# Kernel tuning notes

Hardware: AMD Instinct MI355X
Metric: run time of the kernel (lower is better)

Reference implementation:

```python
import jax, jax.numpy as jnp
import numpy as np

HID = 256        # constant.hidden_size
EMB = 256        # constant.embedding_size
STATE_NUM = 5    # constant.state_num
PAD_ID = 0


def _lstm(x, Wih, Whh, b):
    # x: (N, T, D) -> (N, T, H); single-layer unidirectional, PyTorch gate order i,f,g,o
    N = x.shape[0]
    Hh = Whh.shape[1]
    def step(carry, xt):
        h, c = carry
        g = xt @ Wih.T + h @ Whh.T + b
        i, f, gg, o = jnp.split(g, 4, axis=-1)
        c = jax.nn.sigmoid(f) * c + jax.nn.sigmoid(i) * jnp.tanh(gg)
        h = jax.nn.sigmoid(o) * jnp.tanh(c)
        return (h, c), h
    h0 = jnp.zeros((N, Hh), x.dtype)
    _, ys = jax.lax.scan(step, (h0, h0), jnp.swapaxes(x, 0, 1))
    return jnp.swapaxes(ys, 0, 1)


def setup_inputs() -> dict:
    rng = np.random.RandomState(0)
    B, L, W, V = 8, 128, 48, 50000
    S = STATE_NUM
    P = L // (S - 1)
    batch_utterances = jnp.asarray(rng.randint(0, V, size=(B, L, W)), jnp.int32)
    utterance_sequence_length = jnp.asarray(rng.randint(1, W + 1, size=(B, L)), jnp.int32)
    perm = np.stack([b * L + rng.permutation(L) for b in range(B)]).reshape(-1)
    session_transpose_matrix = jnp.asarray(perm, jnp.int32)
    stm = np.zeros((B, L, S), np.int32)  # col 0 == 0 -> new-state slot (projection path)
    carry = rng.rand(B, L, S - 1) < 0.3
    pos = rng.randint(1, P + 1, size=(B, L, S - 1))
    stm[:, :, 1:] = np.where(carry, -1, pos)
    state_transition_matrix = jnp.asarray(stm)

    def w(*shape):
        return jnp.asarray(rng.randn(*shape) * 0.05, jnp.float32)

    return dict(
        batch_utterances=batch_utterances,
        utterance_sequence_length=utterance_sequence_length,
        session_transpose_matrix=session_transpose_matrix,
        state_transition_matrix=state_transition_matrix,
        max_conversation_length=L,
        emb=w(V, EMB),
        utt_Wih=w(4 * HID, EMB), utt_Whh=w(4 * HID, HID), utt_b=w(4 * HID),
        ws1=w(HID, HID), ws2=w(1, HID),
        conv_Wih=w(4 * HID, HID), conv_Whh=w(4 * HID, HID), conv_b=w(4 * HID),
        sess_Wih=w(4 * HID, HID), sess_Whh=w(4 * HID, HID), sess_b=w(4 * HID),
        Wp=w(HID, 2 * HID), bp=w(HID),
        Ws=w(HID, 2 * HID), bs=w(HID),
    )


def reference(batch_utterances, utterance_sequence_length, session_transpose_matrix,
              state_transition_matrix, max_conversation_length,
              emb, utt_Wih, utt_Whh, utt_b, ws1, ws2,
              conv_Wih, conv_Whh, conv_b, sess_Wih, sess_Whh, sess_b,
              Wp, bp, Ws, bs):
    B, L, W = batch_utterances.shape
    S = STATE_NUM
    P = L // (S - 1)
    Lc = int(max_conversation_length)

    # --- UtteranceEncoder: embedding lookup + word-level LSTM ---
    tok = batch_utterances.reshape(-1, W)            # (B*L, W)
    word_out = _lstm(emb[tok], utt_Wih, utt_Whh, utt_b)  # (B*L, W, H)

    # --- SelfAttentiveEncoder (1 hop) ---
    hbar = jnp.tanh(word_out @ ws1.T)                # (B*L, W, H)
    logits = (hbar @ ws2.T)[..., 0]                  # (B*L, W)
    logits = logits + (-10000.0) * (tok == PAD_ID).astype(logits.dtype)
    alphas = jax.nn.softmax(logits, axis=1)
    att = jnp.einsum('nw,nwh->nh', alphas, word_out).reshape(B, L, HID)

    # --- ConversationEncoder ---
    conv = _lstm(att, conv_Wih, conv_Whh, conv_b)    # (B, L, H)

    # --- SessionEncoder: gather-permute utterances into sessions, LSTM per session ---
    flat = att.reshape(-1, HID)[session_transpose_matrix]       # (B*L, H)
    sess_in = flat.reshape(B * (S - 1), P, HID)
    sess_out = _lstm(sess_in, sess_Wih, sess_Whh, sess_b).reshape(B, S - 1, P, HID)

    # --- StateMatrixEncoder: sequential scatter/gather scan over conversation steps ---
    sess_idx = jnp.clip(jnp.arange(S) - 1, 0, S - 2)            # (S,)
    gathered = sess_out[:, sess_idx]                            # (B, S, P, H)
    conv_shift = jnp.concatenate([conv[:, :1], conv[:, :L - 1]], axis=1)  # conv_repre[i-1] (i==0 -> [0])
    stm_T = jnp.swapaxes(state_transition_matrix, 0, 1)         # (L, B, S)
    cs_T = jnp.swapaxes(conv_shift, 0, 1)                       # (L, B, H)

    def step(prev_row, inp):
        stm_i, cs = inp                                         # (B,S), (B,H)
        posn = jnp.clip(stm_i - 1, 0, P - 1)
        v_g = jnp.take_along_axis(gathered, posn[:, :, None, None], axis=2)[:, :, 0, :]  # (B,S,H)
        is_carry = (stm_i == -1)[..., None]
        is_gather = (stm_i > 0)[..., None]
        v = jnp.where(is_carry, prev_row, jnp.where(is_gather, v_g, 0.0))
        # AvgPool2d((S-1,1)) over exactly S-1 collected vectors == masked mean
        one_res = jnp.sum(jnp.where(stm_i[..., None] != 0, v, 0.0), axis=1) / (S - 1)
        new0 = jax.nn.relu(jnp.concatenate([one_res, cs], axis=-1) @ Wp.T + bp)
        row = jnp.where(is_gather, v_g, 0.0).at[:, 0, :].set(new0)
        return row, row

    _, rows = jax.lax.scan(step, jnp.zeros((B, S, HID), att.dtype), (stm_T, cs_T))
    state_matrix = jnp.swapaxes(rows, 0, 1)                     # (B, L, S, H)

    # --- ScoresCalculator (unidirectional -> LogSoftmax) ---
    uc = jnp.concatenate([att[:, :Lc], conv[:, :Lc]], axis=-1)  # (B, Lc, 2H)
    up = jax.nn.relu(uc @ Ws.T + bs)                            # (B, Lc, H)
    scores = jnp.einsum('blsh,blh->bls', state_matrix[:, :Lc], up)
    return jax.nn.log_softmax(scores, axis=2)
```

## Files before the change

kernel.cpp:

```cpp
#include <hip/hip_runtime.h>
#include <hip/hip_bf16.h>
#include <math.h>

#define HIDN 256
#define GATES 1024
#define LLEN 128
#define WLEN 48
#define SNUM 5
#define PLEN 32
#define EMBD 256

typedef _Float16 f16;
typedef _Float16 h2_t __attribute__((ext_vector_type(2)));
typedef short short8_t __attribute__((ext_vector_type(8)));
typedef float f32x4 __attribute__((ext_vector_type(4)));

__device__ __forceinline__ float sigf(float x){ return 1.0f/(1.0f+expf(-x)); }

__device__ __forceinline__ unsigned short f2bf(float f){
  unsigned int x = __builtin_bit_cast(unsigned int, f);
  x += 0x7fffu + ((x >> 16) & 1u);
  return (unsigned short)(x >> 16);
}
__device__ __forceinline__ float bf2f(unsigned short u){
  unsigned int x = ((unsigned int)u) << 16;
  return __builtin_bit_cast(float, x);
}

__device__ __forceinline__ float fd2(unsigned int w, unsigned int h, float acc){
  h2_t wa = __builtin_bit_cast(h2_t, w);
  h2_t hb = __builtin_bit_cast(h2_t, h);
#if defined(__has_builtin)
#if __has_builtin(__builtin_amdgcn_fdot2)
  return __builtin_amdgcn_fdot2(wa, hb, acc, false);
#else
  return acc + (float)wa[0]*(float)hb[0] + (float)wa[1]*(float)hb[1];
#endif
#else
  return acc + (float)wa[0]*(float)hb[0] + (float)wa[1]*(float)hb[1];
#endif
}
__device__ __forceinline__ float dot8(uint4 w, uint4 h, float acc){
  acc = fd2(w.x, h.x, acc);
  acc = fd2(w.y, h.y, acc);
  acc = fd2(w.z, h.z, acc);
  acc = fd2(w.w, h.w, acc);
  return acc;
}

template<bool GATHER, bool BIAS, bool RELU, bool SPLIT>
__global__ __launch_bounds__(256) void gemm_abt64_k(
  const float* __restrict__ A, const float* __restrict__ A2,
  const float* __restrict__ Bm, const float* __restrict__ bias,
  float* __restrict__ C, const int* __restrict__ gidx,
  int K, int N, int ostride)
{
  __shared__ float As[32][68];
  __shared__ float Bs[32][68];
  const int tid = threadIdx.x;
  const int m0 = blockIdx.x*64, n0 = blockIdx.y*64;
  const int tx = tid & 15, ty = tid >> 4;
  const int lr = tid >> 3;
  const int lc = (tid & 7) * 4;
  float acc[4][4] = {};
  for (int k0 = 0; k0 < K; k0 += 32){
    #pragma unroll
    for (int hf = 0; hf < 2; ++hf){
      const int r = lr + hf*32;
      int am = m0 + r;
      if (GATHER) am = gidx[am];
      const float* asrc;
      if (SPLIT){
        if (k0 < 256) asrc = A  + (size_t)am*256 + k0 + lc;
        else          asrc = A2 + (size_t)am*256 + (k0-256) + lc;
      } else {
        asrc = A + (size_t)am*K + k0 + lc;
      }
      float4 av = *reinterpret_cast<const float4*>(asrc);
      float4 bv = *reinterpret_cast<const float4*>(Bm + (size_t)(n0+r)*K + k0 + lc);
      As[lc+0][r]=av.x; As[lc+1][r]=av.y; As[lc+2][r]=av.z; As[lc+3][r]=av.w;
      Bs[lc+0][r]=bv.x; Bs[lc+1][r]=bv.y; Bs[lc+2][r]=bv.z; Bs[lc+3][r]=bv.w;
    }
    __syncthreads();
    #pragma unroll
    for (int kk = 0; kk < 32; ++kk){
      const float4 a = *reinterpret_cast<const float4*>(&As[kk][ty*4]);
      const float4 b = *reinterpret_cast<const float4*>(&Bs[kk][tx*4]);
      acc[0][0] += a.x*b.x; acc[0][1] += a.x*b.y; acc[0][2] += a.x*b.z; acc[0][3] += a.x*b.w;
      acc[1][0] += a.y*b.x; acc[1][1] += a.y*b.y; acc[1][2] += a.y*b.z; acc[1][3] += a.y*b.w;
      acc[2][0] += a.z*b.x; acc[2][1] += a.z*b.y; acc[2][2] += a.z*b.z; acc[2][3] += a.z*b.w;
      acc[3][0] += a.w*b.x; acc[3][1] += a.w*b.y; acc[3][2] += a.w*b.z; acc[3][3] += a.w*b.w;
    }
    __syncthreads();
  }
  float4 bb;
  if (BIAS) bb = *reinterpret_cast<const float4*>(bias + n0 + tx*4);
  else      { bb.x=0.f; bb.y=0.f; bb.z=0.f; bb.w=0.f; }
  #pragma unroll
  for (int i = 0; i < 4; ++i){
    float4 o;
    o.x = acc[i][0]+bb.x; o.y = acc[i][1]+bb.y; o.z = acc[i][2]+bb.z; o.w = acc[i][3]+bb.w;
    if (RELU){ o.x=fmaxf(o.x,0.f); o.y=fmaxf(o.y,0.f); o.z=fmaxf(o.z,0.f); o.w=fmaxf(o.w,0.f); }
    *reinterpret_cast<float4*>(C + (size_t)(m0+ty*4+i)*ostride + n0 + tx*4) = o;
  }
}

__global__ __launch_bounds__(256) void cvt2_k(
  const float* __restrict__ a, const float* __restrict__ b,
  unsigned short* __restrict__ oa, unsigned short* __restrict__ ob, int n)
{
  for (int i = blockIdx.x*256 + threadIdx.x; i < n; i += gridDim.x*256){
    oa[i] = f2bf(a[i]);
    ob[i] = f2bf(b[i]);
  }
}
__global__ __launch_bounds__(256) void cvt1_k(
  const float* __restrict__ a, unsigned short* __restrict__ o, int n)
{
  for (int i = blockIdx.x*256 + threadIdx.x; i < n; i += gridDim.x*256)
    o[i] = f2bf(a[i]);
}
__global__ __launch_bounds__(256) void cvt_w16_k(
  const float* __restrict__ a, const float* __restrict__ b,
  f16* __restrict__ oa, f16* __restrict__ ob)
{
  const int i = blockIdx.x*256 + threadIdx.x;
  oa[i] = (f16)a[i];
  ob[i] = (f16)b[i];
}

__global__ __launch_bounds__(256) void remap_k(const int* __restrict__ tok, int* __restrict__ gidx2){
  const int idx = blockIdx.x*256 + threadIdx.x;
  const int t = idx >> 10, u = idx & 1023;
  gidx2[idx] = tok[u*WLEN + t];
}

template<int AMODE>
__global__ __launch_bounds__(256) void mmabt_k(
  const void* __restrict__ Asrc, const unsigned short* __restrict__ Wb,
  const float* __restrict__ bias, const int* __restrict__ gidx,
  float* __restrict__ Cout)
{
  __shared__ char As[32768];
  const int tid = threadIdx.x;
  const int w = tid >> 6, l = tid & 63;
  const int lr = l & 15, lg = l >> 4;
  const int m0 = blockIdx.x*64, n0 = blockIdx.y*64;
  #pragma unroll
  for (int q = 0; q < 8; ++q){
    const int ck = tid*8 + q;
    const int rl = ck >> 5, o16 = ck & 31;
    int row = m0 + rl;
    if (AMODE == 1) row = gidx[row];
    char* dst = As + rl*512 + ((o16*16) ^ ((rl & 7) << 4));
    *reinterpret_cast<short8_t*>(dst) = *reinterpret_cast<const short8_t*>(
        (const unsigned short*)Asrc + (size_t)row*256 + o16*8);
  }
  __syncthreads();
  short8_t a[8];
  #pragma unroll
  for (int ks = 0; ks < 8; ++ks){
    const int rl = w*16 + lr;
    a[ks] = *reinterpret_cast<const short8_t*>(As + rl*512 + ((ks*64 + lg*16) ^ ((rl & 7) << 4)));
  }
  #pragma unroll
  for (int nt = 0; nt < 4; ++nt){
    f32x4 acc = f32x4{0,0,0,0};
    const int n = n0 + nt*16 + lr;
    #pragma unroll
    for (int ks = 0; ks < 8; ++ks){
      short8_t b = *reinterpret_cast<const short8_t*>(Wb + (size_t)n*256 + ks*32 + lg*8);
      acc = __builtin_amdgcn_mfma_f32_16x16x32_bf16(a[ks], b, acc, 0, 0, 0);
    }
    const float bn = bias[n];
    #pragma unroll
    for (int r = 0; r < 4; ++r){
      const int m = m0 + w*16 + lg*4 + r;
      Cout[(size_t)m*1024 + n] = acc[r] + bn;
    }
  }
}

__global__ __launch_bounds__(256) void xgemm4_k(
  const float* __restrict__ emb, const unsigned short* __restrict__ Wb,
  const float* __restrict__ bias, const int* __restrict__ gidx,
  unsigned short* __restrict__ Xp)
{
  __shared__ char As[32768];
  const int tid = threadIdx.x;
  const int w = tid >> 6, l = tid & 63;
  const int lr = l & 15, lg = l >> 4;
  const int m0 = blockIdx.x*64;
  const int j0 = blockIdx.y*64;
  #pragma unroll
  for (int q = 0; q < 8; ++q){
    const int ck = tid*8 + q;
    const int rl = ck >> 5, o16 = ck & 31;
    const int row = gidx[m0 + rl];
    const float* src = emb + (size_t)row*256 + o16*8;
    float4 f0 = *reinterpret_cast<const float4*>(src);
    float4 f1 = *reinterpret_cast<const float4*>(src + 4);
    union { short8_t s; unsigned short u[8]; } pk;
    pk.u[0]=f2bf(f0.x); pk.u[1]=f2bf(f0.y); pk.u[2]=f2bf(f0.z); pk.u[3]=f2bf(f0.w);
    pk.u[4]=f2bf(f1.x); pk.u[5]=f2bf(f1.y); pk.u[6]=f2bf(f1.z); pk.u[7]=f2bf(f1.w);
    *reinterpret_cast<short8_t*>(As + rl*512 + ((o16*16) ^ ((rl & 7) << 4))) = pk.s;
  }
  __syncthreads();
  const int jw = j0 + w*16;
  float bs_g[4];
  #pragma unroll
  for (int g = 0; g < 4; ++g) bs_g[g] = bias[g*256 + jw + lr];
  #pragma unroll
  for (int mt = 0; mt < 4; ++mt){
    short8_t a[8];
    const int rl = mt*16 + lr;
    #pragma unroll
    for (int ks = 0; ks < 8; ++ks)
      a[ks] = *reinterpret_cast<const short8_t*>(
          As + rl*512 + ((ks*64 + lg*16) ^ ((rl & 7) << 4)));
    f32x4 acc[4];
    #pragma unroll
    for (int g = 0; g < 4; ++g){
      acc[g] = f32x4{0,0,0,0};
      const unsigned short* wb = Wb + (size_t)(g*256 + jw + lr)*256 + lg*8;
      #pragma unroll
      for (int ks = 0; ks < 8; ++ks){
        short8_t b = *reinterpret_cast<const short8_t*>(wb + ks*32);
        acc[g] = __builtin_amdgcn_mfma_f32_16x16x32_bf16(a[ks], b, acc[g], 0, 0, 0);
      }
    }
    #pragma unroll
    for (int r = 0; r < 4; ++r){
      const int m = m0 + mt*16 + lg*4 + r;
      unsigned long long pk =
          (unsigned long long)f2bf(acc[0][r] + bs_g[0])
        | ((unsigned long long)f2bf(acc[1][r] + bs_g[1]) << 16)
        | ((unsigned long long)f2bf(acc[2][r] + bs_g[2]) << 32)
        | ((unsigned long long)f2bf(acc[3][r] + bs_g[3]) << 48);
      *reinterpret_cast<unsigned long long*>(Xp + (size_t)m*1024 + (jw + lr)*4) = pk;
    }
  }
}

__global__ __launch_bounds__(1024, 1) void word5_k(
  const unsigned short* __restrict__ Xp,
  const unsigned short* __restrict__ Wb,
  unsigned short* __restrict__ woutb)
{
  extern __shared__ char smem[];
  const int tid = threadIdx.x;
  const int w = tid >> 6, l = tid & 63;
  const int lr = l & 15, lg = l >> 4;
  const int S0 = blockIdx.x * 16;
  const int jb = w * 16;
  char* olds = smem + w*8192;
  char* hb0  = smem + 131072;
  char* hb1  = smem + 139264;

  reinterpret_cast<uint4*>(hb0)[tid] = uint4{0,0,0,0};

  #pragma unroll
  for (int q = 0; q < 8; ++q){
    const int ck = l*8 + q;
    const int rl = ck >> 5, o16 = ck & 31;
    short8_t v = *reinterpret_cast<const short8_t*>(
        Wb + (size_t)(768 + jb + rl)*256 + o16*8);
    *reinterpret_cast<short8_t*>(olds + rl*512 + ((o16*16) ^ ((rl & 7) << 4))) = v;
  }
  short8_t wi[8], wf[8];
  #pragma unroll
  for (int ks = 0; ks < 8; ++ks){
    wi[ks] = *reinterpret_cast<const short8_t*>(Wb + (size_t)(      jb + lr)*256 + ks*32 + lg*8);
    wf[ks] = *reinterpret_cast<const short8_t*>(Wb + (size_t)(256 + jb + lr)*256 + ks*32 + lg*8);
  }
  const unsigned short* gbase = Wb + (size_t)(512 + jb + lr)*256 + lg*8;
  float c_reg[4] = {0.f, 0.f, 0.f, 0.f};
  __syncthreads();

  for (int t = 0; t < WLEN; ++t){
    const char* hr = (t & 1) ? hb1 : hb0;
    char* hw = (t & 1) ? hb0 : hb1;
    const unsigned short* pg = gbase;
    asm volatile("" : "+v"(pg));
    unsigned long long xv[4];
    #pragma unroll
    for (int r = 0; r < 4; ++r)
      xv[r] = *reinterpret_cast<const unsigned long long*>(
          Xp + ((size_t)t*1024 + (S0 + lg*4 + r))*1024 + (jb + lr)*4);
    f32x4 aI = f32x4{0,0,0,0}, aF = f32x4{0,0,0,0};
    f32x4 aG = f32x4{0,0,0,0}, aO = f32x4{0,0,0,0};
    #pragma unroll
    for (int ks = 0; ks < 8; ++ks){
      short8_t a = *reinterpret_cast<const short8_t*>(
          hr + lr*512 + ((ks*64 + lg*16) ^ ((lr & 7) << 4)));
      short8_t bg = *reinterpret_cast<const short8_t*>(pg + ks*32);
      short8_t bo = *reinterpret_cast<const short8_t*>(
          olds + lr*512 + ((ks*64 + lg*16) ^ ((lr & 7) << 4)));
      aI = __builtin_amdgcn_mfma_f32_16x16x32_bf16(a, wi[ks], aI, 0, 0, 0);
      aF = __builtin_amdgcn_mfma_f32_16x16x32_bf16(a, wf[ks], aF, 0, 0, 0);
      aG = __builtin_amdgcn_mfma_f32_16x16x32_bf16(a, bg, aG, 0, 0, 0);
      aO = __builtin_amdgcn_mfma_f32_16x16x32_bf16(a, bo, aO, 0, 0, 0);
    }
    const int j = jb + lr;
    #pragma unroll
    for (int r = 0; r < 4; ++r){
      const int s = lg*4 + r;
      float gi = aI[r] + bf2f((unsigned short)(xv[r]));
      float gf = aF[r] + bf2f((unsigned short)(xv[r] >> 16));
      float gg = aG[r] + bf2f((unsigned short)(xv[r] >> 32));
      float go = aO[r] + bf2f((unsigned short)(xv[r] >> 48));
      float cc = sigf(gf)*c_reg[r] + sigf(gi)*tanhf(gg);
      c_reg[r] = cc;
      float hh = sigf(go)*tanhf(cc);
      unsigned short h16 = f2bf(hh);
      woutb[((size_t)(S0+s)*WLEN + t)*256 + j] = h16;
      *reinterpret_cast<unsigned short*>(hw + s*512 + ((j*2) ^ ((s & 7) << 4))) = h16;
    }
    __syncthreads();
  }
}

__global__ __launch_bounds__(1024) void recur3_k(
  const float* __restrict__ xwc, const f16* __restrict__ w16c, float* __restrict__ convb,
  const float* __restrict__ xws, const f16* __restrict__ w16s, float* __restrict__ soutb)
{
  const float* xw; const f16* w16; float* out; int seq, T;
  if (blockIdx.x < 8){ seq = blockIdx.x;     T = 128; xw = xwc; w16 = w16c; out = convb; }
  else               { seq = blockIdx.x - 8; T = 32;  xw = xws; w16 = w16s; out = soutb; }

  extern __shared__ char smem[];
  uint4* w_lds  = (uint4*)smem;
  float* g_s    = (float*)(smem + 131072);
  f16*   h_half = (f16*)(smem + 131072 + 4096);
  const uint4* h4 = (const uint4*)h_half;

  const int tid = threadIdx.x;
  #pragma unroll
  for (int cth = 0; cth < 8; ++cth)
    w_lds[cth*1024 + tid] = *reinterpret_cast<const uint4*>(w16 + (size_t)tid*256 + 192 + cth*8);
  uint4 wr[24];
  #pragma unroll
  for (int cth = 0; cth < 24; ++cth)
    wr[cth] = *reinterpret_cast<const uint4*>(w16 + (size_t)tid*256 + cth*8);
  if (tid < 32) reinterpret_cast<uint4*>(h_half)[tid] = uint4{0,0,0,0};
  float c_reg = 0.f;
  __syncthreads();

  for (int t = 0; t < T; ++t){
    float acc = xw[(size_t)(seq*T + t)*GATES + tid];
    float a0 = 0.f, a1 = 0.f;
    #pragma unroll
    for (int k = 0; k < 24; k += 2){
      const uint4 h0 = h4[k], h1 = h4[k+1];
      a0 = dot8(wr[k],   h0, a0);
      a1 = dot8(wr[k+1], h1, a1);
    }
    #pragma unroll
    for (int cth = 0; cth < 8; cth += 2){
      const uint4 h0 = h4[24+cth], h1 = h4[25+cth];
      a0 = dot8(w_lds[cth*1024 + tid],     h0, a0);
      a1 = dot8(w_lds[(cth+1)*1024 + tid], h1, a1);
    }
    g_s[tid] = acc + a0 + a1;
    __syncthreads();
    if (tid < HIDN){
      const int j = tid;
      float gi = g_s[j], gf = g_s[HIDN+j], gg = g_s[2*HIDN+j], go = g_s[3*HIDN+j];
      float cc = sigf(gf)*c_reg + sigf(gi)*tanhf(gg);
      c_reg = cc;
      float hh = sigf(go)*tanhf(cc);
      h_half[j] = (f16)hh;
      out[(size_t)(seq*T + t)*HIDN + j] = hh;
    }
    __syncthreads();
  }
}

__global__ __launch_bounds__(256) void attlog_k(
  const unsigned short* __restrict__ woutb, const unsigned short* __restrict__ ws1b,
  const float* __restrict__ ws2, float* __restrict__ logits)
{
  const int tid = threadIdx.x;
  const int w = tid >> 6, l = tid & 63;
  const int lr = l & 15, lg = l >> 4;
  const int m0 = blockIdx.x*64;
  short8_t a[8];
  #pragma unroll
  for (int ks = 0; ks < 8; ++ks){
    const int m = m0 + w*16 + lr;
    a[ks] = *reinterpret_cast<const short8_t*>(woutb + (size_t)m*256 + ks*32 + lg*8);
  }
  float part[4] = {0.f, 0.f, 0.f, 0.f};
  #pragma unroll
  for (int nt = 0; nt < 16; ++nt){
    f32x4 acc = f32x4{0,0,0,0};
    const int n = nt*16 + lr;
    #pragma unroll
    for (int ks = 0; ks < 8; ++ks){
      short8_t b = *reinterpret_cast<const short8_t*>(ws1b + (size_t)n*256 + ks*32 + lg*8);
      acc = __builtin_amdgcn_mfma_f32_16x16x32_bf16(a[ks], b, acc, 0, 0, 0);
    }
    const float w2 = ws2[n];
    #pragma unroll
    for (int r = 0; r < 4; ++r) part[r] += w2 * tanhf(acc[r]);
  }
  #pragma unroll
  for (int r = 0; r < 4; ++r){
    float p = part[r];
    p += __shfl_xor(p, 1, 64);
    p += __shfl_xor(p, 2, 64);
    p += __shfl_xor(p, 4, 64);
    p += __shfl_xor(p, 8, 64);
    if (lr == 0) logits[m0 + w*16 + lg*4 + r] = p;
  }
}

__global__ __launch_bounds__(256) void att_softmax_k(
  const unsigned short* __restrict__ woutb, const float* __restrict__ logits,
  const int* __restrict__ tok, float* __restrict__ att, unsigned short* __restrict__ attb)
{
  __shared__ float e[WLEN];
  __shared__ float den_s;
  const int n = blockIdx.x, j = threadIdx.x;
  if (j < WLEN){
    float lgt = logits[n*WLEN + j];
    if (tok[n*WLEN + j] == 0) lgt -= 10000.0f;
    e[j] = lgt;
  }
  __syncthreads();
  if (j == 0){
    float mx = -1e30f;
    for (int ww = 0; ww < WLEN; ++ww) mx = fmaxf(mx, e[ww]);
    float den = 0.f;
    for (int ww = 0; ww < WLEN; ++ww){ float ee = expf(e[ww]-mx); e[ww] = ee; den += ee; }
    den_s = den;
  }
  __syncthreads();
  const float inv = 1.0f/den_s;
  float a = 0.f;
  for (int ww = 0; ww < WLEN; ++ww)
    a += e[ww]*bf2f(woutb[((size_t)n*WLEN + ww)*HIDN + j]);
  a *= inv;
  att[(size_t)n*HIDN + j] = a;
  attb[(size_t)n*HIDN + j] = f2bf(a);
}

__global__ __launch_bounds__(256) void word_gates_k(
    const int* __restrict__ tok, const float* __restrict__ emb,
    const float* __restrict__ Wih, const float* __restrict__ Whh,
    const float* __restrict__ bias, const float* __restrict__ hbuf,
    float* __restrict__ G, int t)
{
  __shared__ float As[32][68];
  __shared__ float Bs[32][68];
  const int tid = threadIdx.x;
  const int m0 = blockIdx.x*64, n0 = blockIdx.y*64;
  const int tx = tid & 15, ty = tid >> 4;
  const int lr = tid >> 3;
  const int lc = (tid & 7) * 4;
  float acc[4][4] = {};
  for (int kt = 0; kt < 16; ++kt){
    const int k0 = (kt & 7)*32;
    const bool xp = (kt < 8);
    #pragma unroll
    for (int hf = 0; hf < 2; ++hf){
      const int r = lr + hf*32;
      float4 av, bv;
      if (xp){
        const int token = tok[(m0+r)*WLEN + t];
        av = *reinterpret_cast<const float4*>(emb + (size_t)token*EMBD + k0 + lc);
      } else {
        av = *reinterpret_cast<const float4*>(hbuf + (size_t)(m0+r)*HIDN + k0 + lc);
      }
      const float* bptr = (xp ? Wih : Whh) + (size_t)(n0+r)*HIDN + k0 + lc;
      bv = *reinterpret_cast<const float4*>(bptr);
      As[lc+0][r]=av.x; As[lc+1][r]=av.y; As[lc+2][r]=av.z; As[lc+3][r]=av.w;
      Bs[lc+0][r]=bv.x; Bs[lc+1][r]=bv.y; Bs[lc+2][r]=bv.z; Bs[lc+3][r]=bv.w;
    }
    __syncthreads();
    #pragma unroll
    for (int kk = 0; kk < 32; ++kk){
      const float4 a = *reinterpret_cast<const float4*>(&As[kk][ty*4]);
      const float4 b = *reinterpret_cast<const float4*>(&Bs[kk][tx*4]);
      acc[0][0] += a.x*b.x; acc[0][1] += a.x*b.y; acc[0][2] += a.x*b.z; acc[0][3] += a.x*b.w;
      acc[1][0] += a.y*b.x; acc[1][1] += a.y*b.y; acc[1][2] += a.y*b.z; acc[1][3] += a.y*b.w;
      acc[2][0] += a.z*b.x; acc[2][1] += a.z*b.y; acc[2][2] += a.z*b.z; acc[2][3] += a.z*b.w;
      acc[3][0] += a.w*b.x; acc[3][1] += a.w*b.y; acc[3][2] += a.w*b.z; acc[3][3] += a.w*b.w;
    }
    __syncthreads();
  }
  const float4 bb = *reinterpret_cast<const float4*>(bias + n0 + tx*4);
  #pragma unroll
  for (int i = 0; i < 4; ++i){
    float4 o;
    o.x = acc[i][0]+bb.x; o.y = acc[i][1]+bb.y; o.z = acc[i][2]+bb.z; o.w = acc[i][3]+bb.w;
    *reinterpret_cast<float4*>(G + (size_t)(m0+ty*4+i)*GATES + n0 + tx*4) = o;
  }
}

__global__ __launch_bounds__(256) void word_update_k(
  const float* __restrict__ G, float* __restrict__ h, float* __restrict__ c,
  unsigned short* __restrict__ woutb, int t)
{
  int idx = blockIdx.x*256 + threadIdx.x;
  int m = idx >> 8, j = idx & 255;
  const float* g = G + (size_t)m*GATES;
  float gi = g[j], gf = g[HIDN+j], gg = g[2*HIDN+j], go = g[3*HIDN+j];
  float cc = c[idx];
  cc = sigf(gf)*cc + sigf(gi)*tanhf(gg);
  float hh = sigf(go)*tanhf(cc);
  c[idx] = cc; h[idx] = hh;
  woutb[(size_t)m*WLEN*HIDN + (size_t)t*HIDN + j] = f2bf(hh);
}

__global__ __launch_bounds__(256) void scan_prep_k(
  const float* __restrict__ sess_out, const float* __restrict__ conv_out,
  const int* __restrict__ stm, float* __restrict__ state, float* __restrict__ onec)
{
  const int bl = blockIdx.x;
  const int b = bl >> 7, l = bl & 127;
  const int j = threadIdx.x;
  float ones = 0.f;
  #pragma unroll
  for (int s = 1; s < SNUM; ++s){
    const int sv = stm[(size_t)bl*SNUM + s];
    float vg = 0.f;
    if (sv > 0){
      int p = sv - 1; if (p > PLEN-1) p = PLEN-1;
      vg = sess_out[((size_t)(b*4 + (s-1))*PLEN + p)*HIDN + j];
    }
    float v = vg;
    if (sv == -1){
      v = 0.f;
      if (l > 0){
        const int pv = stm[(size_t)(bl-1)*SNUM + s];
        if (pv > 0){
          int p2 = pv - 1; if (p2 > PLEN-1) p2 = PLEN-1;
          v = sess_out[((size_t)(b*4 + (s-1))*PLEN + p2)*HIDN + j];
        }
      }
    }
    if (sv != 0) ones += v;
    state[((size_t)bl*SNUM + s)*HIDN + j] = vg;
  }
  onec[(size_t)bl*(2*HIDN) + j] = ones * 0.25f;
  const int lp = (l == 0) ? 0 : (l-1);
  onec[(size_t)bl*(2*HIDN) + HIDN + j] = conv_out[((size_t)(b*LLEN + lp))*HIDN + j];
}

__global__ __launch_bounds__(256) void scores_k(
  const float* __restrict__ state, const float* __restrict__ up, float* __restrict__ out)
{
  const int n = blockIdx.x, j = threadIdx.x;
  __shared__ float red[SNUM][4];
  const float u = up[(size_t)n*HIDN + j];
  const int lane = j & 63, wid = j >> 6;
  #pragma unroll
  for (int s = 0; s < SNUM; ++s){
    float p = state[((size_t)n*SNUM + s)*HIDN + j]*u;
    for (int off = 32; off; off >>= 1) p += __shfl_down(p, off, 64);
    if (lane == 0) red[s][wid] = p;
  }
  __syncthreads();
  if (j == 0){
    float sc[SNUM]; float mx = -1e30f;
    #pragma unroll
    for (int s = 0; s < SNUM; ++s){
      sc[s] = red[s][0]+red[s][1]+red[s][2]+red[s][3];
      mx = fmaxf(mx, sc[s]);
    }
    float den = 0.f;
    #pragma unroll
    for (int s = 0; s < SNUM; ++s) den += expf(sc[s]-mx);
    const float ls = logf(den);
    #pragma unroll
    for (int s = 0; s < SNUM; ++s) out[(size_t)n*SNUM + s] = sc[s]-mx-ls;
  }
}

static const size_t OFF_G     = 0;
static const size_t OFF_H     = OFF_G     + 1048576;
static const size_t OFF_C     = OFF_H     + 262144;
static const size_t OFF_ATT   = OFF_C     + 262144;
static const size_t OFF_ATTB  = OFF_ATT   + 262144;
static const size_t OFF_XWC   = OFF_ATTB  + 131072;
static const size_t OFF_XWS   = OFF_XWC   + 1048576;
static const size_t OFF_CONV  = OFF_XWS   + 1048576;
static const size_t OFF_SOUT  = OFF_CONV  + 262144;
static const size_t OFF_STATE = OFF_SOUT  + 262144;
static const size_t OFF_ONEC  = OFF_STATE + 1310720;
static const size_t OFF_UP    = OFF_ONEC  + 524288;
static const size_t OFF_LOG   = OFF_UP    + 262144;
static const size_t OFF_GIDX2 = OFF_LOG   + 49152;
static const size_t OFF_UWHHB = OFF_GIDX2 + 49152;
static const size_t OFF_WIHB  = OFF_UWHHB + 131072;
static const size_t OFF_WS1B  = OFF_WIHB  + 131072;
static const size_t OFF_CWIHB = OFF_WS1B  + 32768;
static const size_t OFF_SWIHB = OFF_CWIHB + 131072;
static const size_t OFF_W16C  = OFF_SWIHB + 131072;
static const size_t OFF_W16S  = OFF_W16C  + 131072;
static const size_t OFF_WOUTB = OFF_W16S  + 131072;
static const size_t OFF_X     = OFF_WOUTB + 6291456;
static const size_t NEED_X_FLOATS = OFF_X + (size_t)49152*512;

static const size_t WORD_LDS_BYTES  = 131072 + 16384;
static const size_t RECUR_LDS_BYTES = 131072 + 4096 + 512;

extern "C" void kernel_launch(void* const* d_in, const int* in_sizes, int n_in,
                              void* d_out, int out_size, void* d_ws, size_t ws_size,
                              hipStream_t stream)
{
  const int*   tok   = (const int*)  d_in[0];
  const int*   perm  = (const int*)  d_in[2];
  const int*   stm   = (const int*)  d_in[3];
  const float* emb   = (const float*)d_in[5];
  const float* uWih  = (const float*)d_in[6];
  const float* uWhh  = (const float*)d_in[7];
  const float* ub    = (const float*)d_in[8];
  const float* ws1   = (const float*)d_in[9];
  const float* ws2   = (const float*)d_in[10];
  const float* cWih  = (const float*)d_in[11];
  const float* cWhh  = (const float*)d_in[12];
  const float* cb    = (const float*)d_in[13];
  const float* sWih  = (const float*)d_in[14];
  const float* sWhh  = (const float*)d_in[15];
  const float* sb    = (const float*)d_in[16];
  const float* Wp    = (const float*)d_in[17];
  const float* bp    = (const float*)d_in[18];
  const float* Ws    = (const float*)d_in[19];
  const float* bs    = (const float*)d_in[20];

  float* wsf    = (float*)d_ws;
  float* G      = wsf + OFF_G;
  float* h      = wsf + OFF_H;
  float* c      = wsf + OFF_C;
  float* att    = wsf + OFF_ATT;
  float* xwc    = wsf + OFF_XWC;
  float* xws    = wsf + OFF_XWS;
  float* convb  = wsf + OFF_CONV;
  float* soutb  = wsf + OFF_SOUT;
  float* statem = wsf + OFF_STATE;
  float* onec   = wsf + OFF_ONEC;
  float* upb    = wsf + OFF_UP;
  float* logits = wsf + OFF_LOG;
  int*   gidx2  = (int*)(wsf + OFF_GIDX2);
  unsigned short* attb  = (unsigned short*)(wsf + OFF_ATTB);
  unsigned short* uwhhb = (unsigned short*)(wsf + OFF_UWHHB);
  unsigned short* wihb  = (unsigned short*)(wsf + OFF_WIHB);
  unsigned short* ws1b  = (unsigned short*)(wsf + OFF_WS1B);
  unsigned short* cwihb = (unsigned short*)(wsf + OFF_CWIHB);
  unsigned short* swihb = (unsigned short*)(wsf + OFF_SWIHB);
  f16*   w16c   = (f16*)(wsf + OFF_W16C);
  f16*   w16s   = (f16*)(wsf + OFF_W16S);
  unsigned short* woutb = (unsigned short*)(wsf + OFF_WOUTB);
  unsigned short* X16   = (unsigned short*)(wsf + OFF_X);

  const bool useX = ws_size >= NEED_X_FLOATS*sizeof(float);

  hipFuncSetAttribute(reinterpret_cast<const void*>(word5_k),
                      hipFuncAttributeMaxDynamicSharedMemorySize, (int)WORD_LDS_BYTES);
  hipFuncSetAttribute(reinterpret_cast<const void*>(recur3_k),
                      hipFuncAttributeMaxDynamicSharedMemorySize, (int)RECUR_LDS_BYTES);

  cvt2_k<<<256, 256, 0, stream>>>(uWhh, uWih, uwhhb, wihb, 262144);
  cvt2_k<<<256, 256, 0, stream>>>(cWih, sWih, cwihb, swihb, 262144);
  cvt_w16_k<<<1024, 256, 0, stream>>>(cWhh, sWhh, w16c, w16s);
  cvt1_k<<<64, 256, 0, stream>>>(ws1, ws1b, 65536);

  if (useX){
    remap_k<<<192, 256, 0, stream>>>(tok, gidx2);
    xgemm4_k<<<dim3(768,4), 256, 0, stream>>>(emb, wihb, ub, gidx2, X16);
    word5_k<<<64, 1024, WORD_LDS_BYTES, stream>>>(X16, uwhhb, woutb);
  } else {
    hipMemsetAsync(h, 0, 2*262144*sizeof(float), stream);
    for (int t = 0; t < WLEN; ++t){
      word_gates_k<<<dim3(16,16), 256, 0, stream>>>(tok, emb, uWih, uWhh, ub, h, G, t);
      word_update_k<<<1024, 256, 0, stream>>>(G, h, c, woutb, t);
    }
  }

  attlog_k<<<768, 256, 0, stream>>>(woutb, ws1b, ws2, logits);
  att_softmax_k<<<1024, 256, 0, stream>>>(woutb, logits, tok, att, attb);

  mmabt_k<2><<<dim3(16,16), 256, 0, stream>>>(attb, cwihb, cb, nullptr, xwc);
  mmabt_k<1><<<dim3(16,16), 256, 0, stream>>>(attb, swihb, sb, perm, xws);

  recur3_k<<<40, 1024, RECUR_LDS_BYTES, stream>>>(xwc, w16c, convb, xws, w16s, soutb);

  scan_prep_k<<<1024, 256, 0, stream>>>(soutb, convb, stm, statem, onec);
  gemm_abt64_k<false,true,true,false><<<dim3(16,4), 256, 0, stream>>>(
    onec, nullptr, Wp, bp, statem, nullptr, 512, HIDN, SNUM*HIDN);

  gemm_abt64_k<false,true,true,true><<<dim3(16,4), 256, 0, stream>>>(
    att, convb, Ws, bs, upb, nullptr, 512, HIDN, HIDN);
  scores_k<<<1024, 256, 0, stream>>>(statem, upb, (float*)d_out);
}
```

Baseline: 1.170 ms.

## Halve threads in word and recurrent LSTM kernels, two outputs per thread

The word LSTM kernel now runs 512 threads, with each wave covering 32 hidden columns in two 16-column tiles. The forget-gate weights are now streamed from global memory instead of held in registers. The conv/session recurrent kernel also uses 512 threads, each computing two gate rows. Its weights are split across registers, LDS and per-step global/L2 reads, and the next step's input projection is prefetched. The goal is cheaper per-step barriers and less register pressure, at the cost of more serial work per thread and extra memory traffic on every recurrent step.

```diff
diff --git a/kernel.cpp b/kernel.cpp
--- a/kernel.cpp
+++ b/kernel.cpp
@@ -242,7 +242,7 @@
   }
 }
 
-__global__ __launch_bounds__(1024, 1) void word5_k(
+__global__ __launch_bounds__(512, 1) void word6_k(
   const unsigned short* __restrict__ Xp,
   const unsigned short* __restrict__ Wb,
   unsigned short* __restrict__ woutb)
@@ -252,75 +252,84 @@
   const int w = tid >> 6, l = tid & 63;
   const int lr = l & 15, lg = l >> 4;
   const int S0 = blockIdx.x * 16;
-  const int jb = w * 16;
-  char* olds = smem + w*8192;
+  const int jb = w * 32;
+  char* olds = smem + w*16384;
   char* hb0  = smem + 131072;
   char* hb1  = smem + 139264;
 
   reinterpret_cast<uint4*>(hb0)[tid] = uint4{0,0,0,0};
-
-  #pragma unroll
-  for (int q = 0; q < 8; ++q){
-    const int ck = l*8 + q;
+  reinterpret_cast<uint4*>(hb0)[512 + tid] = uint4{0,0,0,0};
+
+  #pragma unroll
+  for (int q = 0; q < 16; ++q){
+    const int ck = l*16 + q;
     const int rl = ck >> 5, o16 = ck & 31;
     short8_t v = *reinterpret_cast<const short8_t*>(
         Wb + (size_t)(768 + jb + rl)*256 + o16*8);
     *reinterpret_cast<short8_t*>(olds + rl*512 + ((o16*16) ^ ((rl & 7) << 4))) = v;
   }
-  short8_t wi[8], wf[8];
-  #pragma unroll
-  for (int ks = 0; ks < 8; ++ks){
-    wi[ks] = *reinterpret_cast<const short8_t*>(Wb + (size_t)(      jb + lr)*256 + ks*32 + lg*8);
-    wf[ks] = *reinterpret_cast<const short8_t*>(Wb + (size_t)(256 + jb + lr)*256 + ks*32 + lg*8);
-  }
+  short8_t wi[2][8];
+  #pragma unroll
+  for (int jt = 0; jt < 2; ++jt)
+    #pragma unroll
+    for (int ks = 0; ks < 8; ++ks)
+      wi[jt][ks] = *reinterpret_cast<const short8_t*>(
+          Wb + (size_t)(jb + jt*16 + lr)*256 + ks*32 + lg*8);
+  const unsigned short* fbase = Wb + (size_t)(256 + jb + lr)*256 + lg*8;
   const unsigned short* gbase = Wb + (size_t)(512 + jb + lr)*256 + lg*8;
-  float c_reg[4] = {0.f, 0.f, 0.f, 0.f};
+  float c_reg[2][4] = {};
   __syncthreads();
 
   for (int t = 0; t < WLEN; ++t){
     const char* hr = (t & 1) ? hb1 : hb0;
     char* hw = (t & 1) ? hb0 : hb1;
+    const unsigned short* pf = fbase;
     const unsigned short* pg = gbase;
-    asm volatile("" : "+v"(pg));
-    unsigned long long xv[4];
-    #pragma unroll
-    for (int r = 0; r < 4; ++r)
-      xv[r] = *reinterpret_cast<const unsigned long long*>(
-          Xp + ((size_t)t*1024 + (S0 + lg*4 + r))*1024 + (jb + lr)*4);
-    f32x4 aI = f32x4{0,0,0,0}, aF = f32x4{0,0,0,0};
-    f32x4 aG = f32x4{0,0,0,0}, aO = f32x4{0,0,0,0};
-    #pragma unroll
-    for (int ks = 0; ks < 8; ++ks){
-      short8_t a = *reinterpret_cast<const short8_t*>(
-          hr + lr*512 + ((ks*64 + lg*16) ^ ((lr & 7) << 4)));
-      short8_t bg = *reinterpret_cast<const short8_t*>(pg + ks*32);
-      short8_t bo = *reinterpret_cast<const short8_t*>(
-          olds + lr*512 + ((ks*64 + lg*16) ^ ((lr & 7) << 4)));
-      aI = __builtin_amdgcn_mfma_f32_16x16x32_bf16(a, wi[ks], aI, 0, 0, 0);
-      aF = __builtin_amdgcn_mfma_f32_16x16x32_bf16(a, wf[ks], aF, 0, 0, 0);
-      aG = __builtin_amdgcn_mfma_f32_16x16x32_bf16(a, bg, aG, 0, 0, 0);
-      aO = __builtin_amdgcn_mfma_f32_16x16x32_bf16(a, bo, aO, 0, 0, 0);
-    }
-    const int j = jb + lr;
-    #pragma unroll
-    for (int r = 0; r < 4; ++r){
-      const int s = lg*4 + r;
-      float gi = aI[r] + bf2f((unsigned short)(xv[r]));
-      float gf = aF[r] + bf2f((unsigned short)(xv[r] >> 16));
-      float gg = aG[r] + bf2f((unsigned short)(xv[r] >> 32));
-      float go = aO[r] + bf2f((unsigned short)(xv[r] >> 48));
-      float cc = sigf(gf)*c_reg[r] + sigf(gi)*tanhf(gg);
-      c_reg[r] = cc;
-      float hh = sigf(go)*tanhf(cc);
-      unsigned short h16 = f2bf(hh);
-      woutb[((size_t)(S0+s)*WLEN + t)*256 + j] = h16;
-      *reinterpret_cast<unsigned short*>(hw + s*512 + ((j*2) ^ ((s & 7) << 4))) = h16;
+    asm volatile("" : "+v"(pf), "+v"(pg));
+    #pragma unroll
+    for (int jt = 0; jt < 2; ++jt){
+      const int j = jb + jt*16 + lr;
+      unsigned long long xv[4];
+      #pragma unroll
+      for (int r = 0; r < 4; ++r)
+        xv[r] = *reinterpret_cast<const unsigned long long*>(
+            Xp + ((size_t)t*1024 + (S0 + lg*4 + r))*1024 + j*4);
+      f32x4 aI = f32x4{0,0,0,0}, aF = f32x4{0,0,0,0};
+      f32x4 aG = f32x4{0,0,0,0}, aO = f32x4{0,0,0,0};
+      #pragma unroll
+      for (int ks = 0; ks < 8; ++ks){
+        short8_t a = *reinterpret_cast<const short8_t*>(
+            hr + lr*512 + ((ks*64 + lg*16) ^ ((lr & 7) << 4)));
+        short8_t bf = *reinterpret_cast<const short8_t*>(pf + (size_t)(jt*16)*256 + ks*32);
+        short8_t bg = *reinterpret_cast<const short8_t*>(pg + (size_t)(jt*16)*256 + ks*32);
+        const int ro = jt*16 + lr;
+        short8_t bo = *reinterpret_cast<const short8_t*>(
+            olds + ro*512 + ((ks*64 + lg*16) ^ ((ro & 7) << 4)));
+        aI = __builtin_amdgcn_mfma_f32_16x16x32_bf16(a, wi[jt][ks], aI, 0, 0, 0);
+        aF = __builtin_amdgcn_mfma_f32_16x16x32_bf16(a, bf, aF, 0, 0, 0);
+        aG = __builtin_amdgcn_mfma_f32_16x16x32_bf16(a, bg, aG, 0, 0, 0);
+        aO = __builtin_amdgcn_mfma_f32_16x16x32_bf16(a, bo, aO, 0, 0, 0);
+      }
+      #pragma unroll
+      for (int r = 0; r < 4; ++r){
+        const int s = lg*4 + r;
+        float gi = aI[r] + bf2f((unsigned short)(xv[r]));
+        float gf = aF[r] + bf2f((unsigned short)(xv[r] >> 16));
+        float gg = aG[r] + bf2f((unsigned short)(xv[r] >> 32));
+        float go = aO[r] + bf2f((unsigned short)(xv[r] >> 48));
+        float cc = sigf(gf)*c_reg[jt][r] + sigf(gi)*tanhf(gg);
+        c_reg[jt][r] = cc;
+        float hh = sigf(go)*tanhf(cc);
+        unsigned short h16 = f2bf(hh);
+        woutb[((size_t)(S0+s)*WLEN + t)*256 + j] = h16;
+        *reinterpret_cast<unsigned short*>(hw + s*512 + ((j*2) ^ ((s & 7) << 4))) = h16;
+      }
     }
     __syncthreads();
   }
 }
 
-__global__ __launch_bounds__(1024) void recur3_k(
+__global__ __launch_bounds__(512, 1) void recur4_k(
   const float* __restrict__ xwc, const f16* __restrict__ w16c, float* __restrict__ convb,
   const float* __restrict__ xws, const f16* __restrict__ w16s, float* __restrict__ soutb)
 {
@@ -335,33 +344,67 @@
   const uint4* h4 = (const uint4*)h_half;
 
   const int tid = threadIdx.x;
-  #pragma unroll
-  for (int cth = 0; cth < 8; ++cth)
-    w_lds[cth*1024 + tid] = *reinterpret_cast<const uint4*>(w16 + (size_t)tid*256 + 192 + cth*8);
+  const int n0 = tid, n1 = tid + 512;
+  #pragma unroll
+  for (int cth = 0; cth < 8; ++cth){
+    w_lds[cth*1024 + n0] = *reinterpret_cast<const uint4*>(w16 + (size_t)n0*256 + 96 + cth*8);
+    w_lds[cth*1024 + n1] = *reinterpret_cast<const uint4*>(w16 + (size_t)n1*256 + 96 + cth*8);
+  }
   uint4 wr[24];
   #pragma unroll
-  for (int cth = 0; cth < 24; ++cth)
-    wr[cth] = *reinterpret_cast<const uint4*>(w16 + (size_t)tid*256 + cth*8);
+  for (int k = 0; k < 12; ++k){
+    wr[k]    = *reinterpret_cast<const uint4*>(w16 + (size_t)n0*256 + k*8);
+    wr[12+k] = *reinterpret_cast<const uint4*>(w16 + (size_t)n1*256 + k*8);
+  }
+  const f16* sb0 = w16 + (size_t)n0*256 + 160;
+  const f16* sb1 = w16 + (size_t)n1*256 + 160;
   if (tid < 32) reinterpret_cast<uint4*>(h_half)[tid] = uint4{0,0,0,0};
   float c_reg = 0.f;
   __syncthreads();
 
+  float xn0 = xw[(size_t)(seq*T)*GATES + n0];
+  float xn1 = xw[(size_t)(seq*T)*GATES + n1];
   for (int t = 0; t < T; ++t){
-    float acc = xw[(size_t)(seq*T + t)*GATES + tid];
-    float a0 = 0.f, a1 = 0.f;
-    #pragma unroll
-    for (int k = 0; k < 24; k += 2){
+    const float acc0 = xn0, acc1 = xn1;
+    if (t + 1 < T){
+      xn0 = xw[(size_t)(seq*T + t + 1)*GATES + n0];
+      xn1 = xw[(size_t)(seq*T + t + 1)*GATES + n1];
+    }
+    const f16* ps0 = sb0;
+    const f16* ps1 = sb1;
+    asm volatile("" : "+v"(ps0), "+v"(ps1));
+    float s0 = 0.f, s1 = 0.f, s2 = 0.f, s3 = 0.f;
+    #pragma unroll
+    for (int k = 0; k < 12; k += 2){
+      uint4 u0 = *reinterpret_cast<const uint4*>(ps0 + k*8);
+      uint4 u1 = *reinterpret_cast<const uint4*>(ps0 + (k+1)*8);
+      uint4 v0 = *reinterpret_cast<const uint4*>(ps1 + k*8);
+      uint4 v1 = *reinterpret_cast<const uint4*>(ps1 + (k+1)*8);
+      const uint4 h0 = h4[20+k], h1 = h4[21+k];
+      s0 = dot8(u0, h0, s0);
+      s1 = dot8(u1, h1, s1);
+      s2 = dot8(v0, h0, s2);
+      s3 = dot8(v1, h1, s3);
+    }
+    float a0 = 0.f, a1 = 0.f, b0 = 0.f, b1 = 0.f;
+    #pragma unroll
+    for (int k = 0; k < 12; k += 2){
       const uint4 h0 = h4[k], h1 = h4[k+1];
-      a0 = dot8(wr[k],   h0, a0);
-      a1 = dot8(wr[k+1], h1, a1);
+      a0 = dot8(wr[k],    h0, a0);
+      a1 = dot8(wr[k+1],  h1, a1);
+      b0 = dot8(wr[12+k], h0, b0);
+      b1 = dot8(wr[13+k], h1, b1);
     }
     #pragma unroll
     for (int cth = 0; cth < 8; cth += 2){
-      const uint4 h0 = h4[24+cth], h1 = h4[25+cth];
-      a0 = dot8(w_lds[cth*1024 + tid],     h0, a0);
-      a1 = dot8(w_lds[(cth+1)*1024 + tid], h1, a1);
-    }
-    g_s[tid] = acc + a0 + a1;
+      const uint4 h0 = h4[12+cth], h1 = h4[13+cth];
+      a0 = dot8(w_lds[cth*1024 + n0],     h0, a0);
+      a1 = dot8(w_lds[(cth+1)*1024 + n0], h1, a1);
+      b0 = dot8(w_lds[cth*1024 + n1],     h0, b0);
+      b1 = dot8(w_lds[(cth+1)*1024 + n1], h1, b1);
+    }
+    g_s[n0] = acc0 + (a0+a1) + (s0+s1);
+    g_s[n1] = acc1 + (b0+b1) + (s2+s3);
     __syncthreads();
     if (tid < HIDN){
       const int j = tid;
@@ -657,9 +700,9 @@
 
   const bool useX = ws_size >= NEED_X_FLOATS*sizeof(float);
 
-  hipFuncSetAttribute(reinterpret_cast<const void*>(word5_k),
+  hipFuncSetAttribute(reinterpret_cast<const void*>(word6_k),
                       hipFuncAttributeMaxDynamicSharedMemorySize, (int)WORD_LDS_BYTES);
-  hipFuncSetAttribute(reinterpret_cast<const void*>(recur3_k),
+  hipFuncSetAttribute(reinterpret_cast<const void*>(recur4_k),
                       hipFuncAttributeMaxDynamicSharedMemorySize, (int)RECUR_LDS_BYTES);
 
   cvt2_k<<<256, 256, 0, stream>>>(uWhh, uWih, uwhhb, wihb, 262144);
@@ -670,7 +713,7 @@
   if (useX){
     remap_k<<<192, 256, 0, stream>>>(tok, gidx2);
     xgemm4_k<<<dim3(768,4), 256, 0, stream>>>(emb, wihb, ub, gidx2, X16);
-    word5_k<<<64, 1024, WORD_LDS_BYTES, stream>>>(X16, uwhhb, woutb);
+    word6_k<<<64, 512, WORD_LDS_BYTES, stream>>>(X16, uwhhb, woutb);
   } else {
     hipMemsetAsync(h, 0, 2*262144*sizeof(float), stream);
     for (int t = 0; t < WLEN; ++t){
@@ -685,7 +728,7 @@
   mmabt_k<2><<<dim3(16,16), 256, 0, stream>>>(attb, cwihb, cb, nullptr, xwc);
   mmabt_k<1><<<dim3(16,16), 256, 0, stream>>>(attb, swihb, sb, perm, xws);
 
-  recur3_k<<<40, 1024, RECUR_LDS_BYTES, stream>>>(xwc, w16c, convb, xws, w16s, soutb);
+  recur4_k<<<40, 512, RECUR_LDS_BYTES, stream>>>(xwc, w16c, convb, xws, w16s, soutb);
 
   scan_prep_k<<<1024, 256, 0, stream>>>(soutb, convb, stm, statem, onec);
   gemm_abt64_k<false,true,true,false><<<dim3(16,4), 256, 0, stream>>>(
```

After: 1.705 ms. +45.8%, slower.

## Stream i/f recurrent weights from global with double-buffered prefetch; fold token remap into GEMM

Applied to the files above, without the earlier changes.

The word-level LSTM kernel stops holding the input and forget gate weight fragments in registers for the whole sequence. Each step now streams the i, f and g weights from global/L2 with a two-deep register prefetch ahead of the MFMAs, which frees VGPRs but adds global loads inside the recurrent loop. Separately, the token transpose kernel is removed and its index computation is done inline in the embedding GEMM, saving one launch and a small workspace buffer.

```diff
diff --git a/kernel.cpp b/kernel.cpp
--- a/kernel.cpp
+++ b/kernel.cpp
@@ -129,12 +129,6 @@
   ob[i] = (f16)b[i];
 }
 
-__global__ __launch_bounds__(256) void remap_k(const int* __restrict__ tok, int* __restrict__ gidx2){
-  const int idx = blockIdx.x*256 + threadIdx.x;
-  const int t = idx >> 10, u = idx & 1023;
-  gidx2[idx] = tok[u*WLEN + t];
-}
-
 template<int AMODE>
 __global__ __launch_bounds__(256) void mmabt_k(
   const void* __restrict__ Asrc, const unsigned short* __restrict__ Wb,
@@ -183,7 +177,7 @@
 
 __global__ __launch_bounds__(256) void xgemm4_k(
   const float* __restrict__ emb, const unsigned short* __restrict__ Wb,
-  const float* __restrict__ bias, const int* __restrict__ gidx,
+  const float* __restrict__ bias, const int* __restrict__ tok,
   unsigned short* __restrict__ Xp)
 {
   __shared__ char As[32768];
@@ -196,7 +190,9 @@
   for (int q = 0; q < 8; ++q){
     const int ck = tid*8 + q;
     const int rl = ck >> 5, o16 = ck & 31;
-    const int row = gidx[m0 + rl];
+    const int m = m0 + rl;
+    const int tt = m >> 10, uu = m & 1023;
+    const int row = tok[uu*WLEN + tt];
     const float* src = emb + (size_t)row*256 + o16*8;
     float4 f0 = *reinterpret_cast<const float4*>(src);
     float4 f1 = *reinterpret_cast<const float4*>(src + 4);
@@ -242,7 +238,7 @@
   }
 }
 
-__global__ __launch_bounds__(1024, 1) void word5_k(
+__global__ __launch_bounds__(1024, 1) void word7_k(
   const unsigned short* __restrict__ Xp,
   const unsigned short* __restrict__ Wb,
   unsigned short* __restrict__ woutb)
@@ -267,12 +263,8 @@
         Wb + (size_t)(768 + jb + rl)*256 + o16*8);
     *reinterpret_cast<short8_t*>(olds + rl*512 + ((o16*16) ^ ((rl & 7) << 4))) = v;
   }
-  short8_t wi[8], wf[8];
-  #pragma unroll
-  for (int ks = 0; ks < 8; ++ks){
-    wi[ks] = *reinterpret_cast<const short8_t*>(Wb + (size_t)(      jb + lr)*256 + ks*32 + lg*8);
-    wf[ks] = *reinterpret_cast<const short8_t*>(Wb + (size_t)(256 + jb + lr)*256 + ks*32 + lg*8);
-  }
+  const unsigned short* ibase = Wb + (size_t)(      jb + lr)*256 + lg*8;
+  const unsigned short* fbase = Wb + (size_t)(256 + jb + lr)*256 + lg*8;
   const unsigned short* gbase = Wb + (size_t)(512 + jb + lr)*256 + lg*8;
   float c_reg[4] = {0.f, 0.f, 0.f, 0.f};
   __syncthreads();
@@ -280,25 +272,39 @@
   for (int t = 0; t < WLEN; ++t){
     const char* hr = (t & 1) ? hb1 : hb0;
     char* hw = (t & 1) ? hb0 : hb1;
+    const unsigned short* pi = ibase;
+    const unsigned short* pf = fbase;
     const unsigned short* pg = gbase;
-    asm volatile("" : "+v"(pg));
+    asm volatile("" : "+v"(pi), "+v"(pf), "+v"(pg));
     unsigned long long xv[4];
     #pragma unroll
     for (int r = 0; r < 4; ++r)
       xv[r] = *reinterpret_cast<const unsigned long long*>(
           Xp + ((size_t)t*1024 + (S0 + lg*4 + r))*1024 + (jb + lr)*4);
+    short8_t bi[2], bf[2], bg[2];
+    bi[0] = *reinterpret_cast<const short8_t*>(pi);
+    bf[0] = *reinterpret_cast<const short8_t*>(pf);
+    bg[0] = *reinterpret_cast<const short8_t*>(pg);
+    bi[1] = *reinterpret_cast<const short8_t*>(pi + 32);
+    bf[1] = *reinterpret_cast<const short8_t*>(pf + 32);
+    bg[1] = *reinterpret_cast<const short8_t*>(pg + 32);
     f32x4 aI = f32x4{0,0,0,0}, aF = f32x4{0,0,0,0};
     f32x4 aG = f32x4{0,0,0,0}, aO = f32x4{0,0,0,0};
     #pragma unroll
     for (int ks = 0; ks < 8; ++ks){
       short8_t a = *reinterpret_cast<const short8_t*>(
           hr + lr*512 + ((ks*64 + lg*16) ^ ((lr & 7) << 4)));
-      short8_t bg = *reinterpret_cast<const short8_t*>(pg + ks*32);
       short8_t bo = *reinterpret_cast<const short8_t*>(
           olds + lr*512 + ((ks*64 + lg*16) ^ ((lr & 7) << 4)));
-      aI = __builtin_amdgcn_mfma_f32_16x16x32_bf16(a, wi[ks], aI, 0, 0, 0);
-      aF = __builtin_amdgcn_mfma_f32_16x16x32_bf16(a, wf[ks], aF, 0, 0, 0);
-      aG = __builtin_amdgcn_mfma_f32_16x16x32_bf16(a, bg, aG, 0, 0, 0);
+      const short8_t ci = bi[ks & 1], cf = bf[ks & 1], cg = bg[ks & 1];
+      if (ks + 2 < 8){
+        bi[ks & 1] = *reinterpret_cast<const short8_t*>(pi + (ks+2)*32);
+        bf[ks & 1] = *reinterpret_cast<const short8_t*>(pf + (ks+2)*32);
+        bg[ks & 1] = *reinterpret_cast<const short8_t*>(pg + (ks+2)*32);
+      }
+      aI = __builtin_amdgcn_mfma_f32_16x16x32_bf16(a, ci, aI, 0, 0, 0);
+      aF = __builtin_amdgcn_mfma_f32_16x16x32_bf16(a, cf, aF, 0, 0, 0);
+      aG = __builtin_amdgcn_mfma_f32_16x16x32_bf16(a, cg, aG, 0, 0, 0);
       aO = __builtin_amdgcn_mfma_f32_16x16x32_bf16(a, bo, aO, 0, 0, 0);
     }
     const int j = jb + lr;
@@ -591,8 +597,7 @@
 static const size_t OFF_ONEC  = OFF_STATE + 1310720;
 static const size_t OFF_UP    = OFF_ONEC  + 524288;
 static const size_t OFF_LOG   = OFF_UP    + 262144;
-static const size_t OFF_GIDX2 = OFF_LOG   + 49152;
-static const size_t OFF_UWHHB = OFF_GIDX2 + 49152;
+static const size_t OFF_UWHHB = OFF_LOG   + 49152;
 static const size_t OFF_WIHB  = OFF_UWHHB + 131072;
 static const size_t OFF_WS1B  = OFF_WIHB  + 131072;
 static const size_t OFF_CWIHB = OFF_WS1B  + 32768;
@@ -643,7 +648,6 @@
   float* onec   = wsf + OFF_ONEC;
   float* upb    = wsf + OFF_UP;
   float* logits = wsf + OFF_LOG;
-  int*   gidx2  = (int*)(wsf + OFF_GIDX2);
   unsigned short* attb  = (unsigned short*)(wsf + OFF_ATTB);
   unsigned short* uwhhb = (unsigned short*)(wsf + OFF_UWHHB);
   unsigned short* wihb  = (unsigned short*)(wsf + OFF_WIHB);
@@ -657,7 +661,7 @@
 
   const bool useX = ws_size >= NEED_X_FLOATS*sizeof(float);
 
-  hipFuncSetAttribute(reinterpret_cast<const void*>(word5_k),
+  hipFuncSetAttribute(reinterpret_cast<const void*>(word7_k),
                       hipFuncAttributeMaxDynamicSharedMemorySize, (int)WORD_LDS_BYTES);
   hipFuncSetAttribute(reinterpret_cast<const void*>(recur3_k),
                       hipFuncAttributeMaxDynamicSharedMemorySize, (int)RECUR_LDS_BYTES);
@@ -668,9 +672,8 @@
   cvt1_k<<<64, 256, 0, stream>>>(ws1, ws1b, 65536);
 
   if (useX){
-    remap_k<<<192, 256, 0, stream>>>(tok, gidx2);
-    xgemm4_k<<<dim3(768,4), 256, 0, stream>>>(emb, wihb, ub, gidx2, X16);
-    word5_k<<<64, 1024, WORD_LDS_BYTES, stream>>>(X16, uwhhb, woutb);
+    xgemm4_k<<<dim3(768,4), 256, 0, stream>>>(emb, wihb, ub, tok, X16);
+    word7_k<<<64, 1024, WORD_LDS_BYTES, stream>>>(X16, uwhhb, woutb);
   } else {
     hipMemsetAsync(h, 0, 2*262144*sizeof(float), stream);
     for (int t = 0; t < WLEN; ++t){
```

After: 1.386 ms. +18.5%, slower.
